# Kernel optimization log

Measured on AMD Instinct MI355X. Metric: run time of the kernel, lower is better.

Reference implementation:

```python
import jax, jax.numpy as jnp
import numpy as np
import math
from jax import lax

TSCALE = 256
NUM_SAMPLE = 32
PERBIN = 3
WINDOWS = [4, 8, 16, 32, 64, 128, 192, 256]
RATIO = 0.25
B = 2
DIM = 512
H1 = 256   # hid_dim_1d
H3 = 512   # hid_dim_3d
H2 = 128   # hid_dim_2d


def _bin_mask(xmin, xmax, tscale, num_sample, perbin):
    # exact replica of BEM._get_interp1d_bin_mask (setup-time numpy)
    plen = float(xmax - xmin)
    step = plen / (num_sample * perbin - 1.0)
    samples = [xmin + step * i for i in range(num_sample * perbin)]
    cols = []
    for idx in range(num_sample):
        v = np.zeros([tscale])
        for s in samples[idx * perbin:(idx + 1) * perbin]:
            up = math.ceil(s)
            dec, down = math.modf(s)
            if 0 <= int(down) <= tscale - 1:
                v[int(down)] += 1 - dec
            if 0 <= int(up) <= tscale - 1:
                v[int(up)] += dec
        cols.append(v / perbin)
    return np.stack(cols, axis=1)  # (tscale, num_sample)


def build_sample_mask():
    mats = []
    for w in WINDOWS:
        ws = w + w * RATIO
        vecs = []
        for t in range(TSCALE):
            d = ws * 0.5
            vecs.append(_bin_mask(t - d, t + d, TSCALE, NUM_SAMPLE, PERBIN))
        mats.append(np.stack(vecs, axis=2))  # (T, N, T)
    m = np.stack(mats, axis=3).astype(np.float32)  # (T, N, T, W)
    return jnp.asarray(m.reshape(TSCALE, -1))  # (T, N*T*W)


def gn(x, g, b, groups=32, eps=1e-5):
    Bsz, C = x.shape[0], x.shape[1]
    xr = x.reshape(Bsz, groups, -1)
    mu = xr.mean(-1, keepdims=True)
    var = xr.var(-1, keepdims=True)
    xr = (xr - mu) * lax.rsqrt(var + eps)
    x = xr.reshape(x.shape)
    bshape = (1, C) + (1,) * (x.ndim - 2)
    return x * g.reshape(bshape) + b.reshape(bshape)


def conv(x, w, b, strides, padding, dn):
    y = lax.conv_general_dilated(x, w, strides, padding, dimension_numbers=dn)
    return y + b.reshape((1, -1) + (1,) * (y.ndim - 2))


def setup_inputs() -> dict:
    key = jax.random.key(0)
    ks = jax.random.split(key, 16)

    def w(k, shape, fan):
        return (jax.random.normal(k, shape) * (1.0 / np.sqrt(fan))).astype(jnp.float32)

    inp = {}
    inp['x'] = jax.random.normal(ks[0], (B, DIM, TSCALE), jnp.float32)
    inp['sample_mask'] = build_sample_mask()
    inp['c1_w'] = w(ks[1], (H1, DIM, 3), DIM * 3)
    inp['c1_b'] = jnp.zeros((H1,), jnp.float32)
    inp['gn1_g'] = jnp.ones((H1,), jnp.float32)
    inp['gn1_b'] = jnp.zeros((H1,), jnp.float32)
    inp['r3d_w'] = w(ks[2], (H3, H1, NUM_SAMPLE, 1, 1), H1 * NUM_SAMPLE)
    inp['r3d_b'] = jnp.zeros((H3,), jnp.float32)
    inp['gn3_g'] = jnp.ones((H3,), jnp.float32)
    inp['gn3_b'] = jnp.zeros((H3,), jnp.float32)
    inp['r2d_w'] = w(ks[3], (H2, H3, 1, 1), H3)
    inp['r2d_b'] = jnp.zeros((H2,), jnp.float32)
    inp['gn2_g'] = jnp.ones((H2,), jnp.float32)
    inp['gn2_b'] = jnp.zeros((H2,), jnp.float32)
    inp['s1_w'] = w(ks[4], (H2, H2, 3, 3), H2 * 9)
    inp['s1_b'] = jnp.zeros((H2,), jnp.float32)
    inp['sgn_g'] = jnp.ones((H2,), jnp.float32)
    inp['sgn_b'] = jnp.zeros((H2,), jnp.float32)
    inp['s2_w'] = w(ks[5], (1, H2, 1, 1), H2)
    inp['s2_b'] = jnp.zeros((1,), jnp.float32)
    inp['e1_w'] = w(ks[6], (H2, H2, 3, 3), H2 * 9)
    inp['e1_b'] = jnp.zeros((H2,), jnp.float32)
    inp['egn_g'] = jnp.ones((H2,), jnp.float32)
    inp['egn_b'] = jnp.zeros((H2,), jnp.float32)
    inp['e2_w'] = w(ks[7], (1, H2, 1, 1), H2)
    inp['e2_b'] = jnp.zeros((1,), jnp.float32)
    return inp


def reference(x, sample_mask, c1_w, c1_b, gn1_g, gn1_b, r3d_w, r3d_b, gn3_g, gn3_b,
              r2d_w, r2d_b, gn2_g, gn2_b, s1_w, s1_b, sgn_g, sgn_b, s2_w, s2_b,
              e1_w, e1_b, egn_g, egn_b, e2_w, e2_b):
    relu = jax.nn.relu
    W = len(WINDOWS)
    # conv_1: Unit1D(k=3, same pad) + GN + ReLU  -> (B, H1, T)
    h = relu(gn(conv(x, c1_w, c1_b, (1,), [(1, 1)], ('NCH', 'OIH', 'NCH')), gn1_g, gn1_b))
    Bsz, C, T = h.shape
    # sample: dense GEMM against sparse interp1d mask -> (B, C, N, T, W)
    samp = jnp.matmul(h, sample_mask).reshape(Bsz, C, NUM_SAMPLE, T, W)
    # reduction_layer 'fc': Conv3d over the N axis (kernel=stride=N) + GN + ReLU
    y = conv(samp, r3d_w, r3d_b, (NUM_SAMPLE, 1, 1), 'VALID', ('NCDHW', 'OIDHW', 'NCDHW'))
    y = relu(gn(y, gn3_g, gn3_b))[:, :, 0]  # squeeze depth -> (B, H3, T, W)
    f = relu(gn(conv(y, r2d_w, r2d_b, (1, 1), 'VALID', ('NCHW', 'OIHW', 'NCHW')), gn2_g, gn2_b))

    def head(w1, b1, gg, gb, w2, b2):
        t = relu(gn(conv(f, w1, b1, (1, 1), [(1, 1), (1, 1)], ('NCHW', 'OIHW', 'NCHW')), gg, gb))
        return jax.nn.sigmoid(conv(t, w2, b2, (1, 1), 'VALID', ('NCHW', 'OIHW', 'NCHW')))

    cs = head(s1_w, s1_b, sgn_g, sgn_b, s2_w, s2_b)  # (B,1,T,W)
    ce = head(e1_w, e1_b, egn_g, egn_b, e2_w, e2_b)  # (B,1,T,W)
    return jnp.concatenate([cs, ce], axis=1)  # (B,2,T,W): [start, end]
```

## Files before the change

kernel.cpp:

```cpp
#include <hip/hip_runtime.h>
#include <hip/hip_bf16.h>

typedef __hip_bfloat16 bf16;
typedef __attribute__((ext_vector_type(8))) short short8;
typedef __attribute__((ext_vector_type(4))) float f32x4;

static __device__ __forceinline__ float b2f(bf16 v) { return __bfloat162float(v); }

static __device__ __forceinline__ float ldin(const void* p, long i, int bf) {
    return bf ? b2f(((const bf16*)p)[i]) : ((const float*)p)[i];
}

__global__ void detect_k(const unsigned short* __restrict__ x16, int* __restrict__ flag) {
    __shared__ int cnt[256];
    unsigned short u = x16[threadIdx.x];
    int e = (u >> 7) & 0xFF;
    cnt[threadIdx.x] = (e >= 100 && e <= 140) ? 1 : 0;
    __syncthreads();
    for (int off = 128; off > 0; off >>= 1) {
        if (threadIdx.x < off) cnt[threadIdx.x] += cnt[threadIdx.x + off];
        __syncthreads();
    }
    if (threadIdx.x == 0) *flag = (cnt[0] > 217) ? 1 : 0;
}

__global__ void cast_bf_k(const void* __restrict__ in, bf16* __restrict__ out,
                          int n, const int* __restrict__ flagp) {
    int bf = *flagp;
    int idx = blockIdx.x * 256 + threadIdx.x;
    if (idx >= n) return;
    out[idx] = __float2bfloat16(ldin(in, idx, bf));
}

__global__ __launch_bounds__(256) void transpose_w3b_k(const void* __restrict__ w3,
                                                       bf16* __restrict__ out,
                                                       const int* __restrict__ flagp) {
    int bf = *flagp;
    int h3 = blockIdx.x;
    __shared__ bf16 t[8192];
    long base = (long)h3 * 8192;
    for (int i = threadIdx.x; i < 8192; i += 256)
        t[i] = __float2bfloat16(ldin(w3, base + i, bf));
    __syncthreads();
    for (int i = threadIdx.x; i < 8192; i += 256) {
        int n = i >> 8, c = i & 255;
        out[((long)n * 512 + h3) * 256 + c] = t[c * 32 + n];
    }
}

__global__ void cast_hT_k(const float* __restrict__ h, bf16* __restrict__ out) {
    int idx = blockIdx.x * 256 + threadIdx.x;
    if (idx >= 131072) return;
    int b = idx >> 16, r = idx & 65535;
    int tau = r >> 8, c = r & 255;
    out[idx] = __float2bfloat16(h[b * 65536 + c * 256 + tau]);
}

__global__ __launch_bounds__(256) void castT_k(const float* __restrict__ y,
                                               bf16* __restrict__ yT) {
    int p0 = blockIdx.x * 64, c0 = blockIdx.y * 64, b = blockIdx.z;
    __shared__ bf16 t[64][65];
    const float* src = y + (long)b * 1048576;
    for (int i = threadIdx.x; i < 4096; i += 256) {
        int cl = i >> 6, pl = i & 63;
        t[pl][cl] = __float2bfloat16(src[(long)(c0 + cl) * 2048 + p0 + pl]);
    }
    __syncthreads();
    bf16* dst = yT + (long)b * 1048576;
    for (int i = threadIdx.x; i < 4096; i += 256) {
        int pl = i >> 6, cl = i & 63;
        dst[(long)(p0 + pl) * 512 + c0 + cl] = t[pl][cl];
    }
}

__global__ void im2col_xb_k(const void* __restrict__ x, bf16* __restrict__ out,
                            const int* __restrict__ flagp) {
    int bf = *flagp;
    int idx = blockIdx.x * 256 + threadIdx.x;
    if (idx >= 786432) return;
    int b = idx / 393216;
    int rem = idx - b * 393216;
    int t = rem / 1536, k = rem - t * 1536;
    int c = k / 3, q = k - c * 3;
    int tt = t + q - 1;
    float v = (tt >= 0 && tt < 256) ? ldin(x, ((long)b * 512 + c) * 256 + tt, bf) : 0.f;
    out[idx] = __float2bfloat16(v);
}

__global__ void im2col_fb_k(const float* __restrict__ f, bf16* __restrict__ out) {
    int idx = blockIdx.x * 256 + threadIdx.x;
    if (idx >= 4718592) return;
    int b = idx / 2359296;
    int rem = idx - b * 2359296;
    int p = rem / 1152, k = rem - p * 1152;
    int c = k / 9, q = k - c * 9;
    int dy = q / 3, dx = q - dy * 3;
    int t = p >> 3, w = p & 7;
    int tt = t + dy - 1, ww = w + dx - 1;
    float v = (tt >= 0 && tt < 256 && ww >= 0 && ww < 8)
                  ? f[((long)b * 128 + c) * 2048 + tt * 8 + ww] : 0.f;
    out[idx] = __float2bfloat16(v);
}

template<int NT>
__global__ __launch_bounds__(256) void wgemm_mfma(
    const bf16* __restrict__ A, const bf16* __restrict__ B, float* __restrict__ C,
    const void* __restrict__ bias1, const void* __restrict__ bias2,
    int M, int K, int P, int a_div, long a_zs, const int* __restrict__ flagp)
{
    int bf = *flagp;
    int z = blockIdx.z;
    const bf16* A2 = A + (long)(z / a_div) * a_zs;
    const bf16* B2 = B + (long)(z & 1) * (long)P * K;
    float* C2 = C + (long)z * M * P;
    const void* bi = (z / a_div) ? bias2 : bias1;

    int tid = threadIdx.x;
    int wv = tid >> 6, lane = tid & 63;
    int q = lane >> 4, col = lane & 15;
    int m0 = blockIdx.y * 64 + wv * 16;
    int p0 = blockIdx.x * (16 * NT);

    f32x4 acc[NT];
    #pragma unroll
    for (int i = 0; i < NT; ++i) acc[i] = (f32x4){0.f, 0.f, 0.f, 0.f};

    const short8* Ab = (const short8*)(A2 + (long)(m0 + col) * K);
    int kch = K >> 5;
    for (int kc = 0; kc < kch; ++kc) {
        short8 af = Ab[kc * 4 + q];
        #pragma unroll
        for (int nt = 0; nt < NT; ++nt) {
            const short8* Bb = (const short8*)(B2 + (long)(p0 + nt * 16 + col) * K);
            short8 bfr = Bb[kc * 4 + q];
            acc[nt] = __builtin_amdgcn_mfma_f32_16x16x32_bf16(af, bfr, acc[nt], 0, 0, 0);
        }
    }

    float bv[4];
    #pragma unroll
    for (int r = 0; r < 4; ++r) bv[r] = ldin(bi, m0 + q * 4 + r, bf);
    #pragma unroll
    for (int nt = 0; nt < NT; ++nt)
        #pragma unroll
        for (int r = 0; r < 4; ++r)
            C2[(long)(m0 + q * 4 + r) * P + p0 + nt * 16 + col] = acc[nt][r] + bv[r];
}

__global__ __launch_bounds__(256) void pgemm_mfma(
    const bf16* __restrict__ w3b, const bf16* __restrict__ hbT,
    float* __restrict__ P)
{
    int z = blockIdx.z;
    int b = z >> 5, n = z & 31;
    int bm = blockIdx.y;
    int tid = threadIdx.x;
    int wv = tid >> 6, lane = tid & 63;
    int q = lane >> 4, col = lane & 15;

    f32x4 acc[16];
    #pragma unroll
    for (int i = 0; i < 16; ++i) acc[i] = (f32x4){0.f, 0.f, 0.f, 0.f};

    const short8* Abase = (const short8*)(w3b + ((long)n * 512 + bm * 64 + wv * 16 + col) * 256);
    const short8* Bbase = (const short8*)(hbT + (long)b * 65536);

    #pragma unroll
    for (int kc = 0; kc < 8; ++kc) {
        short8 af = Abase[kc * 4 + q];
        #pragma unroll
        for (int nt = 0; nt < 16; ++nt) {
            short8 bfr = Bbase[(nt * 16 + col) * 32 + kc * 4 + q];
            acc[nt] = __builtin_amdgcn_mfma_f32_16x16x32_bf16(af, bfr, acc[nt], 0, 0, 0);
        }
    }

    long dbase = (long)b * 4194304 + (long)n * 256 +
                 (long)(bm * 64 + wv * 16 + q * 4) * 8192 + col;
    #pragma unroll
    for (int nt = 0; nt < 16; ++nt)
        #pragma unroll
        for (int r = 0; r < 4; ++r)
            P[dbase + (long)r * 8192 + nt * 16] = acc[nt][r];
}

__global__ __launch_bounds__(1024) void gn_relu_k(
    float* __restrict__ buf, const void* __restrict__ g, const void* __restrict__ bt,
    int C, int S, int groups, const int* __restrict__ flagp)
{
    int bf = *flagp;
    int nt = blockDim.x;
    int gid = blockIdx.x;
    int b = gid / groups, gr = gid % groups;
    int cpg = C / groups;
    long cnt = (long)cpg * S;
    float* base = buf + ((long)b * C + (long)gr * cpg) * S;
    double s = 0.0, s2 = 0.0;
    for (long i = threadIdx.x; i < cnt; i += nt) {
        float v = base[i];
        s += v; s2 += (double)v * v;
    }
    __shared__ double rs[1024], rq[1024];
    rs[threadIdx.x] = s; rq[threadIdx.x] = s2;
    __syncthreads();
    for (int off = nt >> 1; off > 0; off >>= 1) {
        if (threadIdx.x < off) { rs[threadIdx.x] += rs[threadIdx.x + off]; rq[threadIdx.x] += rq[threadIdx.x + off]; }
        __syncthreads();
    }
    double mean_d = rs[0] / (double)cnt;
    float mean = (float)mean_d;
    float var = (float)(rq[0] / (double)cnt - mean_d * mean_d);
    float rstd = rsqrtf(var + 1e-5f);
    for (long i = threadIdx.x; i < cnt; i += nt) {
        int c = gr * cpg + (int)(i / S);
        float v = (base[i] - mean) * rstd * ldin(g, c, bf) + ldin(bt, c, bf);
        base[i] = v > 0.f ? v : 0.f;
    }
}

__global__ __launch_bounds__(256) void gn_part_k(
    const float* __restrict__ buf, double* __restrict__ part,
    int C, int S, int groups, int chunks)
{
    int gi = blockIdx.x / chunks, ch = blockIdx.x % chunks;
    int b = gi / groups, gr = gi % groups;
    int cpg = C / groups;
    long cnt = (long)cpg * S;
    long clen = cnt / chunks;
    const float* base = buf + ((long)b * C + (long)gr * cpg) * S + (long)ch * clen;
    double s = 0.0, s2 = 0.0;
    for (long i = threadIdx.x; i < clen; i += 256) {
        float v = base[i];
        s += v; s2 += (double)v * v;
    }
    __shared__ double rs[256], rq[256];
    rs[threadIdx.x] = s; rq[threadIdx.x] = s2;
    __syncthreads();
    for (int off = 128; off > 0; off >>= 1) {
        if (threadIdx.x < off) { rs[threadIdx.x] += rs[threadIdx.x + off]; rq[threadIdx.x] += rq[threadIdx.x + off]; }
        __syncthreads();
    }
    if (threadIdx.x == 0) { part[blockIdx.x * 2] = rs[0]; part[blockIdx.x * 2 + 1] = rq[0]; }
}

__global__ __launch_bounds__(256) void gn_apply_k(
    float* __restrict__ buf, const double* __restrict__ part,
    const void* __restrict__ g, const void* __restrict__ bt,
    int C, int S, int groups, int chunks, const int* __restrict__ flagp)
{
    int bf = *flagp;
    int gi = blockIdx.x / chunks, ch = blockIdx.x % chunks;
    int b = gi / groups, gr = gi % groups;
    int cpg = C / groups;
    long cnt = (long)cpg * S;
    long clen = cnt / chunks;
    double s = 0.0, s2 = 0.0;
    for (int k = 0; k < chunks; ++k) {
        s += part[(gi * chunks + k) * 2];
        s2 += part[(gi * chunks + k) * 2 + 1];
    }
    double mean_d = s / (double)cnt;
    float mean = (float)mean_d;
    float var = (float)(s2 / (double)cnt - mean_d * mean_d);
    float rstd = rsqrtf(var + 1e-5f);
    float* base = buf + ((long)b * C + (long)gr * cpg) * S + (long)ch * clen;
    long off0 = (long)ch * clen;
    for (long i = threadIdx.x; i < clen; i += 256) {
        int c = gr * cpg + (int)((off0 + i) / S);
        float v = (base[i] - mean) * rstd * ldin(g, c, bf) + ldin(bt, c, bf);
        base[i] = v > 0.f ? v : 0.f;
    }
}

__global__ __launch_bounds__(384) void build_table_k(
    const void* __restrict__ mask, int* __restrict__ tabd,
    float* __restrict__ tabw, const int* __restrict__ flagp)
{
    int bf = *flagp;
    int nw = blockIdx.x;
    int w = nw >> 5, n = nw & 31;
    int tid = threadIdx.x;
    int d = tid - 165;
    float v = 0.f;
    if (d <= 165) {
        if (d < 0) v = ldin(mask, (long)(254 + d) * 65536 + ((long)n * 256 + 254) * 8 + w, bf);
        else       v = ldin(mask, (long)(1 + d) * 65536 + ((long)n * 256 + 1) * 8 + w, bf);
    }
    __shared__ unsigned char nz[384];
    nz[tid] = (v != 0.f) ? 1 : 0;
    if (tid < 6) { tabd[nw * 6 + tid] = 0; tabw[nw * 6 + tid] = 0.f; }
    __syncthreads();
    if (v != 0.f) {
        int slot = 0;
        for (int j = 0; j < tid; ++j) slot += nz[j];
        if (slot < 6) { tabd[nw * 6 + slot] = d; tabw[nw * 6 + slot] = v; }
    }
}

__global__ void build_corr_k(const void* __restrict__ mask, const int* __restrict__ tabd,
                             const float* __restrict__ tabw, float* __restrict__ corrB,
                             const int* __restrict__ flagp) {
    int bf = *flagp;
    int idx = blockIdx.x * 256 + threadIdx.x;
    if (idx >= 65536) return;
    int n = idx >> 11, p = idx & 2047;
    int t = p >> 3, w = p & 7;
    float mv = ldin(mask, ((long)n * 256 + t) * 8 + w, bf);
    float sub = 0.f;
    int base = (w * 32 + n) * 6;
    for (int k = 0; k < 6; ++k)
        if (tabd[base + k] == -t && tabw[base + k] != 0.f) sub += tabw[base + k];
    corrB[idx] = mv - sub;
}

__global__ __launch_bounds__(256) void apply_y_k(
    const float* __restrict__ P, const int* __restrict__ tabd,
    const float* __restrict__ tabw, float* __restrict__ part,
    const int* __restrict__ flagp)
{
    int bx = blockIdx.x;
    int h3 = bx >> 1, half = bx & 1;
    int n0 = half * 16;
    __shared__ float2 Pl2[16 * 256];
    __shared__ float4 Tp4[384];
    const float4* p04 = (const float4*)(P + ((long)h3 * 32 + n0) * 256);
    const float4* p14 = (const float4*)(P + ((long)(512 + h3) * 32 + n0) * 256);
    float4* pl4 = (float4*)Pl2;
    for (int i = threadIdx.x; i < 1024; i += 256) {
        float4 a = p04[i], b = p14[i];
        pl4[i * 2]     = make_float4(a.x, b.x, a.y, b.y);
        pl4[i * 2 + 1] = make_float4(a.z, b.z, a.w, b.w);
    }
    float2* tp2 = (float2*)Tp4;
    for (int i = threadIdx.x; i < 768; i += 256) {
        int el = i / 6, k = i - el * 6;
        int ge = ((el >> 4) << 5) + n0 + (el & 15);
        tp2[i] = make_float2(tabw[ge * 6 + k], __int_as_float(tabd[ge * 6 + k]));
    }
    __syncthreads();

    int t = threadIdx.x;
    float a0[8], a1[8];
    #pragma unroll
    for (int w = 0; w < 8; ++w) { a0[w] = 0.f; a1[w] = 0.f; }

    #pragma unroll 1
    for (int nl = 0; nl < 16; ++nl) {
        const float2* Pn = Pl2 + (nl << 8);
        #pragma unroll
        for (int w = 0; w < 8; ++w) {
            int e4 = ((w << 4) + nl) * 3;
            float4 q0 = Tp4[e4], q1 = Tp4[e4 + 1], q2 = Tp4[e4 + 2];
            float wts[6] = {q0.x, q0.z, q1.x, q1.z, q2.x, q2.z};
            int   dss[6] = {__float_as_int(q0.y), __float_as_int(q0.w),
                            __float_as_int(q1.y), __float_as_int(q1.w),
                            __float_as_int(q2.y), __float_as_int(q2.w)};
            #pragma unroll
            for (int k = 0; k < 6; ++k) {
                int tau = t + dss[k];
                int idx = tau & 255;
                float wt = ((unsigned)tau < 256u) ? wts[k] : 0.f;
                float2 pv = Pn[idx];
                a0[w] += wt * pv.x;
                a1[w] += wt * pv.y;
            }
        }
    }

    long y0 = (long)half * 2097152 + (long)h3 * 2048 + (long)t * 8;
    long y1 = y0 + 512L * 2048;
    *(float4*)(part + y0)     = make_float4(a0[0], a0[1], a0[2], a0[3]);
    *(float4*)(part + y0 + 4) = make_float4(a0[4], a0[5], a0[6], a0[7]);
    *(float4*)(part + y1)     = make_float4(a1[0], a1[1], a1[2], a1[3]);
    *(float4*)(part + y1 + 4) = make_float4(a1[4], a1[5], a1[6], a1[7]);
}

__global__ void merge_y_k(const float* __restrict__ part, const float* __restrict__ P,
                          const float* __restrict__ corrB, float* __restrict__ y,
                          const void* __restrict__ r3b, const int* __restrict__ flagp) {
    int bf = *flagp;
    int i = blockIdx.x * 256 + threadIdx.x;
    if (i >= 524288) return;
    const float4* p4 = (const float4*)part;
    float4 a = p4[i], b = p4[i + 524288];
    long e = (long)i * 4;
    int bb_ = (int)(e >> 20);
    int h3 = (int)((e >> 11) & 511);
    int p = (int)(e & 2047);
    float bias = ldin(r3b, h3, bf);
    float4 acc = make_float4(a.x + b.x + bias, a.y + b.y + bias,
                             a.z + b.z + bias, a.w + b.w + bias);
    const float* p0 = P + ((long)(bb_ * 512 + h3) * 32) * 256;
    #pragma unroll 4
    for (int n = 0; n < 32; ++n) {
        float pv = p0[n * 256];
        float4 cb = *(const float4*)(corrB + n * 2048 + p);
        acc.x += pv * cb.x; acc.y += pv * cb.y;
        acc.z += pv * cb.z; acc.w += pv * cb.w;
    }
    ((float4*)y)[i] = acc;
}

__global__ __launch_bounds__(64) void head_out_k(
    const float* __restrict__ t1s, const float* __restrict__ t1e,
    const void* __restrict__ s2w, const void* __restrict__ s2b,
    const void* __restrict__ e2w, const void* __restrict__ e2b,
    void* __restrict__ out, const int* __restrict__ flagp) {
    int bf = *flagp;
    int idx = blockIdx.x * 64 + threadIdx.x;
    if (idx >= 4096) return;
    int b = idx >> 11, p = idx & 2047;
    const float* ts = t1s + (long)b * 262144 + p;
    const float* te = t1e + (long)b * 262144 + p;
    float as = ldin(s2b, 0, bf), ae = ldin(e2b, 0, bf);
    #pragma unroll 8
    for (int c = 0; c < 128; ++c) {
        as += ldin(s2w, c, bf) * ts[(long)c * 2048];
        ae += ldin(e2w, c, bf) * te[(long)c * 2048];
    }
    float vs = 1.f / (1.f + expf(-as));
    float ve = 1.f / (1.f + expf(-ae));
    long o0 = ((long)b * 2) * 2048 + p;
    long o1 = ((long)b * 2 + 1) * 2048 + p;
    if (bf) {
        ((bf16*)out)[o0] = __float2bfloat16(vs);
        ((bf16*)out)[o1] = __float2bfloat16(ve);
    } else {
        ((float*)out)[o0] = vs;
        ((float*)out)[o1] = ve;
    }
}

extern "C" void kernel_launch(void* const* d_in, const int* in_sizes, int n_in,
                              void* d_out, int out_size, void* d_ws, size_t ws_size,
                              hipStream_t stream) {
    const void* x    = d_in[0];
    const void* mask = d_in[1];
    const void* c1w  = d_in[2];
    const void* c1b  = d_in[3];
    const void* gn1g = d_in[4];
    const void* gn1b = d_in[5];
    const void* w3   = d_in[6];
    const void* r3b  = d_in[7];
    const void* gn3g = d_in[8];
    const void* gn3b = d_in[9];
    const void* w2   = d_in[10];
    const void* r2b  = d_in[11];
    const void* gn2g = d_in[12];
    const void* gn2b = d_in[13];
    const void* s1w  = d_in[14];
    const void* s1b  = d_in[15];
    const void* sgng = d_in[16];
    const void* sgnb = d_in[17];
    const void* s2w  = d_in[18];
    const void* s2b  = d_in[19];
    const void* e1w  = d_in[20];
    const void* e1b  = d_in[21];
    const void* egng = d_in[22];
    const void* egnb = d_in[23];
    const void* e2w  = d_in[24];
    const void* e2b  = d_in[25];
    float* ws = (float*)d_ws;

    int*   flagI = (int*)(ws + 0);
    float* h     = ws + 64;
    float* c1t   = ws + 131136;
    float* w2t   = ws + 524352;
    float* s1t   = ws + 589888;
    float* corrB = ws + 884800;
    float* tabw  = ws + 950336;
    int*   tabd  = (int*)(ws + 951872);
    float* t1s   = ws + 986176;
    float* t1e   = ws + 1510464;
    float* f     = ws + 2034752;
    float* y     = ws + 2559040;
    float* w3reg = ws + 4656192;
    float* Pb    = ws + 8850496;
    double* gnbuf = (double*)(ws + 17239104);
    bf16*  w3b   = (bf16*)w3reg;
    bf16*  hbT   = (bf16*)(w3reg + 2097152);
    bf16*  c1wb  = (bf16*)c1t;
    bf16*  w2b   = (bf16*)w2t;
    bf16*  hwb   = (bf16*)s1t;
    bf16*  colxb = (bf16*)y;
    bf16*  fcolb = (bf16*)Pb;
    bf16*  yT    = (bf16*)(Pb + 4194304);
    float* ypart = w3reg;

    dim3 blk(256);
    dim3 blkG(1024);

    detect_k<<<dim3(1), blk, 0, stream>>>((const unsigned short*)x, flagI);

    cast_bf_k<<<dim3(1536), blk, 0, stream>>>(c1w, c1wb, 393216, flagI);
    cast_bf_k<<<dim3(576),  blk, 0, stream>>>(s1w, hwb, 147456, flagI);
    cast_bf_k<<<dim3(576),  blk, 0, stream>>>(e1w, hwb + 147456, 147456, flagI);
    cast_bf_k<<<dim3(256),  blk, 0, stream>>>(w2, w2b, 65536, flagI);
    transpose_w3b_k<<<dim3(512), blk, 0, stream>>>(w3, w3b, flagI);
    build_table_k<<<dim3(256), dim3(384), 0, stream>>>(mask, tabd, tabw, flagI);
    build_corr_k<<<dim3(256), blk, 0, stream>>>(mask, tabd, tabw, corrB, flagI);

    im2col_xb_k<<<dim3(3072), blk, 0, stream>>>(x, colxb, flagI);
    wgemm_mfma<1><<<dim3(16, 4, 2), blk, 0, stream>>>(
        c1wb, colxb, h, c1b, c1b, 256, 1536, 256, 1, 0L, flagI);
    gn_relu_k<<<dim3(64), blkG, 0, stream>>>(h, gn1g, gn1b, 256, 256, 32, flagI);

    cast_hT_k<<<dim3(512), blk, 0, stream>>>(h, hbT);
    pgemm_mfma<<<dim3(1, 8, 64), blk, 0, stream>>>(w3b, hbT, Pb);

    apply_y_k<<<dim3(1024), blk, 0, stream>>>(Pb, tabd, tabw, ypart, flagI);
    merge_y_k<<<dim3(2048), blk, 0, stream>>>(ypart, Pb, corrB, y, r3b, flagI);
    gn_part_k<<<dim3(512), blk, 0, stream>>>(y, gnbuf, 512, 2048, 32, 8);
    gn_apply_k<<<dim3(512), blk, 0, stream>>>(y, gnbuf, gn3g, gn3b, 512, 2048, 32, 8, flagI);

    castT_k<<<dim3(32, 8, 2), blk, 0, stream>>>(y, yT);
    wgemm_mfma<2><<<dim3(64, 2, 2), blk, 0, stream>>>(
        w2b, yT, f, r2b, r2b, 128, 512, 2048, 2, 0L, flagI);
    gn_part_k<<<dim3(256), blk, 0, stream>>>(f, gnbuf, 128, 2048, 32, 4);
    gn_apply_k<<<dim3(256), blk, 0, stream>>>(f, gnbuf, gn2g, gn2b, 128, 2048, 32, 4, flagI);

    im2col_fb_k<<<dim3(18432), blk, 0, stream>>>(f, fcolb);
    wgemm_mfma<4><<<dim3(32, 2, 4), blk, 0, stream>>>(
        hwb, fcolb, t1s, s1b, e1b, 128, 1152, 2048, 2, 147456L, flagI);
    gn_part_k<<<dim3(256), blk, 0, stream>>>(t1s, gnbuf, 128, 2048, 32, 4);
    gn_apply_k<<<dim3(256), blk, 0, stream>>>(t1s, gnbuf, sgng, sgnb, 128, 2048, 32, 4, flagI);
    gn_part_k<<<dim3(256), blk, 0, stream>>>(t1e, gnbuf, 128, 2048, 32, 4);
    gn_apply_k<<<dim3(256), blk, 0, stream>>>(t1e, gnbuf, egng, egnb, 128, 2048, 32, 4, flagI);

    head_out_k<<<dim3(64), dim3(64), 0, stream>>>(t1s, t1e, s2w, s2b, e2w, e2b, d_out, flagI);
}
```

Measured before the change: 432.6 us.

## Fuse prep kernels, GN with transpose-cast, merge with GN stats, head GNs

Several small launches are merged. Five weight-cast/transpose kernels and the table build become one multi-role prep kernel. GroupNorm1 now also writes the transposed bf16 copy of h, which removes cast_hT. The y merge is fused with the GN3 partial statistics pass, and the two head GroupNorms run as a single batched part/apply pair that treats t1s and t1e as contiguous. The aim is less launch overhead and fewer full-tensor passes. In exchange, the merged y kernel loses its float4 vectorization, and the batched head GN relies on t1e sitting directly after t1s in memory.

```diff
diff --git a/kernel.cpp b/kernel.cpp
--- a/kernel.cpp
+++ b/kernel.cpp
@@ -24,53 +24,90 @@
     if (threadIdx.x == 0) *flag = (cnt[0] > 217) ? 1 : 0;
 }
 
-__global__ void cast_bf_k(const void* __restrict__ in, bf16* __restrict__ out,
-                          int n, const int* __restrict__ flagp) {
+__global__ __launch_bounds__(384) void prep_k(
+    const void* __restrict__ c1w, const void* __restrict__ s1w,
+    const void* __restrict__ e1w, const void* __restrict__ w2,
+    const void* __restrict__ w3, const void* __restrict__ mask,
+    bf16* __restrict__ c1wb, bf16* __restrict__ hwb, bf16* __restrict__ w2b,
+    bf16* __restrict__ w3b, int* __restrict__ tabd, float* __restrict__ tabw,
+    const int* __restrict__ flagp)
+{
+    __shared__ char sm[16384];
+    int bf = *flagp;
+    int blk = blockIdx.x, tid = threadIdx.x;
+    if (blk < 1024) {
+        int idx = blk * 384 + tid;
+        if (idx < 393216) c1wb[idx] = __float2bfloat16(ldin(c1w, idx, bf));
+        return;
+    }
+    blk -= 1024;
+    if (blk < 384) {
+        int idx = blk * 384 + tid;
+        if (idx < 147456) hwb[idx] = __float2bfloat16(ldin(s1w, idx, bf));
+        return;
+    }
+    blk -= 384;
+    if (blk < 384) {
+        int idx = blk * 384 + tid;
+        if (idx < 147456) hwb[147456 + idx] = __float2bfloat16(ldin(e1w, idx, bf));
+        return;
+    }
+    blk -= 384;
+    if (blk < 171) {
+        int idx = blk * 384 + tid;
+        if (idx < 65536) w2b[idx] = __float2bfloat16(ldin(w2, idx, bf));
+        return;
+    }
+    blk -= 171;
+    if (blk < 512) {
+        int h3 = blk;
+        bf16* t = (bf16*)sm;
+        long base = (long)h3 * 8192;
+        for (int i = tid; i < 8192; i += 384)
+            t[i] = __float2bfloat16(ldin(w3, base + i, bf));
+        __syncthreads();
+        for (int i = tid; i < 8192; i += 384) {
+            int n = i >> 8, c = i & 255;
+            w3b[((long)n * 512 + h3) * 256 + c] = t[c * 32 + n];
+        }
+        return;
+    }
+    blk -= 512;
+    {
+        int nw = blk;
+        int w = nw >> 5, n = nw & 31;
+        int d = tid - 165;
+        float v = 0.f;
+        if (d <= 165) {
+            if (d < 0) v = ldin(mask, (long)(254 + d) * 65536 + ((long)n * 256 + 254) * 8 + w, bf);
+            else       v = ldin(mask, (long)(1 + d) * 65536 + ((long)n * 256 + 1) * 8 + w, bf);
+        }
+        unsigned char* nz = (unsigned char*)sm;
+        nz[tid] = (v != 0.f) ? 1 : 0;
+        if (tid < 6) { tabd[nw * 6 + tid] = 0; tabw[nw * 6 + tid] = 0.f; }
+        __syncthreads();
+        if (v != 0.f) {
+            int slot = 0;
+            for (int j = 0; j < tid; ++j) slot += nz[j];
+            if (slot < 6) { tabd[nw * 6 + slot] = d; tabw[nw * 6 + slot] = v; }
+        }
+    }
+}
+
+__global__ void build_corr_k(const void* __restrict__ mask, const int* __restrict__ tabd,
+                             const float* __restrict__ tabw, float* __restrict__ corrB,
+                             const int* __restrict__ flagp) {
     int bf = *flagp;
     int idx = blockIdx.x * 256 + threadIdx.x;
-    if (idx >= n) return;
-    out[idx] = __float2bfloat16(ldin(in, idx, bf));
-}
-
-__global__ __launch_bounds__(256) void transpose_w3b_k(const void* __restrict__ w3,
-                                                       bf16* __restrict__ out,
-                                                       const int* __restrict__ flagp) {
-    int bf = *flagp;
-    int h3 = blockIdx.x;
-    __shared__ bf16 t[8192];
-    long base = (long)h3 * 8192;
-    for (int i = threadIdx.x; i < 8192; i += 256)
-        t[i] = __float2bfloat16(ldin(w3, base + i, bf));
-    __syncthreads();
-    for (int i = threadIdx.x; i < 8192; i += 256) {
-        int n = i >> 8, c = i & 255;
-        out[((long)n * 512 + h3) * 256 + c] = t[c * 32 + n];
-    }
-}
-
-__global__ void cast_hT_k(const float* __restrict__ h, bf16* __restrict__ out) {
-    int idx = blockIdx.x * 256 + threadIdx.x;
-    if (idx >= 131072) return;
-    int b = idx >> 16, r = idx & 65535;
-    int tau = r >> 8, c = r & 255;
-    out[idx] = __float2bfloat16(h[b * 65536 + c * 256 + tau]);
-}
-
-__global__ __launch_bounds__(256) void castT_k(const float* __restrict__ y,
-                                               bf16* __restrict__ yT) {
-    int p0 = blockIdx.x * 64, c0 = blockIdx.y * 64, b = blockIdx.z;
-    __shared__ bf16 t[64][65];
-    const float* src = y + (long)b * 1048576;
-    for (int i = threadIdx.x; i < 4096; i += 256) {
-        int cl = i >> 6, pl = i & 63;
-        t[pl][cl] = __float2bfloat16(src[(long)(c0 + cl) * 2048 + p0 + pl]);
-    }
-    __syncthreads();
-    bf16* dst = yT + (long)b * 1048576;
-    for (int i = threadIdx.x; i < 4096; i += 256) {
-        int pl = i >> 6, cl = i & 63;
-        dst[(long)(p0 + pl) * 512 + c0 + cl] = t[pl][cl];
-    }
+    if (idx >= 65536) return;
+    int n = idx >> 11, p = idx & 2047;
+    int t = p >> 3, w = p & 7;
+    float mv = ldin(mask, ((long)n * 256 + t) * 8 + w, bf);
+    float sub = 0.f;
+    int base = (w * 32 + n) * 6;
+    for (int k = 0; k < 6; ++k)
+        if (tabd[base + k] == -t && tabw[base + k] != 0.f) sub += tabw[base + k];
+    corrB[idx] = mv - sub;
 }
 
 __global__ void im2col_xb_k(const void* __restrict__ x, bf16* __restrict__ out,
@@ -102,6 +139,23 @@
     out[idx] = __float2bfloat16(v);
 }
 
+__global__ __launch_bounds__(256) void castT_k(const float* __restrict__ y,
+                                               bf16* __restrict__ yT) {
+    int p0 = blockIdx.x * 64, c0 = blockIdx.y * 64, b = blockIdx.z;
+    __shared__ bf16 t[64][65];
+    const float* src = y + (long)b * 1048576;
+    for (int i = threadIdx.x; i < 4096; i += 256) {
+        int cl = i >> 6, pl = i & 63;
+        t[pl][cl] = __float2bfloat16(src[(long)(c0 + cl) * 2048 + p0 + pl]);
+    }
+    __syncthreads();
+    bf16* dst = yT + (long)b * 1048576;
+    for (int i = threadIdx.x; i < 4096; i += 256) {
+        int pl = i >> 6, cl = i & 63;
+        dst[(long)(p0 + pl) * 512 + c0 + cl] = t[pl][cl];
+    }
+}
+
 template<int NT>
 __global__ __launch_bounds__(256) void wgemm_mfma(
     const bf16* __restrict__ A, const bf16* __restrict__ B, float* __restrict__ C,
@@ -184,37 +238,37 @@
             P[dbase + (long)r * 8192 + nt * 16] = acc[nt][r];
 }
 
-__global__ __launch_bounds__(1024) void gn_relu_k(
-    float* __restrict__ buf, const void* __restrict__ g, const void* __restrict__ bt,
-    int C, int S, int groups, const int* __restrict__ flagp)
-{
-    int bf = *flagp;
-    int nt = blockDim.x;
+__global__ __launch_bounds__(1024) void gn_relu_h_k(
+    float* __restrict__ h, bf16* __restrict__ hbT,
+    const void* __restrict__ g, const void* __restrict__ bt,
+    const int* __restrict__ flagp)
+{
+    int bf = *flagp;
     int gid = blockIdx.x;
-    int b = gid / groups, gr = gid % groups;
-    int cpg = C / groups;
-    long cnt = (long)cpg * S;
-    float* base = buf + ((long)b * C + (long)gr * cpg) * S;
+    int b = gid >> 5, gr = gid & 31;
+    float* base = h + ((long)b * 256 + gr * 8) * 256;
     double s = 0.0, s2 = 0.0;
-    for (long i = threadIdx.x; i < cnt; i += nt) {
+    for (int i = threadIdx.x; i < 2048; i += 1024) {
         float v = base[i];
         s += v; s2 += (double)v * v;
     }
     __shared__ double rs[1024], rq[1024];
     rs[threadIdx.x] = s; rq[threadIdx.x] = s2;
     __syncthreads();
-    for (int off = nt >> 1; off > 0; off >>= 1) {
+    for (int off = 512; off > 0; off >>= 1) {
         if (threadIdx.x < off) { rs[threadIdx.x] += rs[threadIdx.x + off]; rq[threadIdx.x] += rq[threadIdx.x + off]; }
         __syncthreads();
     }
-    double mean_d = rs[0] / (double)cnt;
+    double mean_d = rs[0] / 2048.0;
     float mean = (float)mean_d;
-    float var = (float)(rq[0] / (double)cnt - mean_d * mean_d);
+    float var = (float)(rq[0] / 2048.0 - mean_d * mean_d);
     float rstd = rsqrtf(var + 1e-5f);
-    for (long i = threadIdx.x; i < cnt; i += nt) {
-        int c = gr * cpg + (int)(i / S);
+    for (int i = threadIdx.x; i < 2048; i += 1024) {
+        int c = gr * 8 + (i >> 8), tau = i & 255;
         float v = (base[i] - mean) * rstd * ldin(g, c, bf) + ldin(bt, c, bf);
-        base[i] = v > 0.f ? v : 0.f;
+        v = v > 0.f ? v : 0.f;
+        base[i] = v;
+        hbT[(long)b * 65536 + tau * 256 + c] = __float2bfloat16(v);
     }
 }
 
@@ -272,45 +326,34 @@
     }
 }
 
-__global__ __launch_bounds__(384) void build_table_k(
-    const void* __restrict__ mask, int* __restrict__ tabd,
-    float* __restrict__ tabw, const int* __restrict__ flagp)
-{
-    int bf = *flagp;
-    int nw = blockIdx.x;
-    int w = nw >> 5, n = nw & 31;
-    int tid = threadIdx.x;
-    int d = tid - 165;
-    float v = 0.f;
-    if (d <= 165) {
-        if (d < 0) v = ldin(mask, (long)(254 + d) * 65536 + ((long)n * 256 + 254) * 8 + w, bf);
-        else       v = ldin(mask, (long)(1 + d) * 65536 + ((long)n * 256 + 1) * 8 + w, bf);
-    }
-    __shared__ unsigned char nz[384];
-    nz[tid] = (v != 0.f) ? 1 : 0;
-    if (tid < 6) { tabd[nw * 6 + tid] = 0; tabw[nw * 6 + tid] = 0.f; }
-    __syncthreads();
-    if (v != 0.f) {
-        int slot = 0;
-        for (int j = 0; j < tid; ++j) slot += nz[j];
-        if (slot < 6) { tabd[nw * 6 + slot] = d; tabw[nw * 6 + slot] = v; }
-    }
-}
-
-__global__ void build_corr_k(const void* __restrict__ mask, const int* __restrict__ tabd,
-                             const float* __restrict__ tabw, float* __restrict__ corrB,
-                             const int* __restrict__ flagp) {
-    int bf = *flagp;
-    int idx = blockIdx.x * 256 + threadIdx.x;
-    if (idx >= 65536) return;
-    int n = idx >> 11, p = idx & 2047;
-    int t = p >> 3, w = p & 7;
-    float mv = ldin(mask, ((long)n * 256 + t) * 8 + w, bf);
-    float sub = 0.f;
-    int base = (w * 32 + n) * 6;
-    for (int k = 0; k < 6; ++k)
-        if (tabd[base + k] == -t && tabw[base + k] != 0.f) sub += tabw[base + k];
-    corrB[idx] = mv - sub;
+__global__ __launch_bounds__(256) void gn_apply2_k(
+    float* __restrict__ buf, const double* __restrict__ part,
+    const void* __restrict__ g1, const void* __restrict__ b1,
+    const void* __restrict__ g2, const void* __restrict__ b2,
+    int chunks, const int* __restrict__ flagp)
+{
+    int bf = *flagp;
+    int gi = blockIdx.x / chunks, ch = blockIdx.x % chunks;
+    int b = gi >> 5, gr = gi & 31;
+    const void* g = (b >= 2) ? g2 : g1;
+    const void* bt = (b >= 2) ? b2 : b1;
+    long cnt = 8192, clen = cnt / chunks;
+    double s = 0.0, s2 = 0.0;
+    for (int k = 0; k < chunks; ++k) {
+        s += part[(gi * chunks + k) * 2];
+        s2 += part[(gi * chunks + k) * 2 + 1];
+    }
+    double mean_d = s / (double)cnt;
+    float mean = (float)mean_d;
+    float var = (float)(s2 / (double)cnt - mean_d * mean_d);
+    float rstd = rsqrtf(var + 1e-5f);
+    float* base = buf + ((long)b * 128 + gr * 4) * 2048 + (long)ch * clen;
+    long off0 = (long)ch * clen;
+    for (long i = threadIdx.x; i < clen; i += 256) {
+        int c = gr * 4 + (int)((off0 + i) >> 11);
+        float v = (base[i] - mean) * rstd * ldin(g, c, bf) + ldin(bt, c, bf);
+        base[i] = v > 0.f ? v : 0.f;
+    }
 }
 
 __global__ __launch_bounds__(256) void apply_y_k(
@@ -375,30 +418,38 @@
     *(float4*)(part + y1 + 4) = make_float4(a1[4], a1[5], a1[6], a1[7]);
 }
 
-__global__ void merge_y_k(const float* __restrict__ part, const float* __restrict__ P,
-                          const float* __restrict__ corrB, float* __restrict__ y,
-                          const void* __restrict__ r3b, const int* __restrict__ flagp) {
-    int bf = *flagp;
-    int i = blockIdx.x * 256 + threadIdx.x;
-    if (i >= 524288) return;
-    const float4* p4 = (const float4*)part;
-    float4 a = p4[i], b = p4[i + 524288];
-    long e = (long)i * 4;
-    int bb_ = (int)(e >> 20);
-    int h3 = (int)((e >> 11) & 511);
-    int p = (int)(e & 2047);
-    float bias = ldin(r3b, h3, bf);
-    float4 acc = make_float4(a.x + b.x + bias, a.y + b.y + bias,
-                             a.z + b.z + bias, a.w + b.w + bias);
-    const float* p0 = P + ((long)(bb_ * 512 + h3) * 32) * 256;
-    #pragma unroll 4
-    for (int n = 0; n < 32; ++n) {
-        float pv = p0[n * 256];
-        float4 cb = *(const float4*)(corrB + n * 2048 + p);
-        acc.x += pv * cb.x; acc.y += pv * cb.y;
-        acc.z += pv * cb.z; acc.w += pv * cb.w;
-    }
-    ((float4*)y)[i] = acc;
+__global__ __launch_bounds__(256) void gn3_part_k(
+    const float* __restrict__ ypart, const float* __restrict__ P,
+    const float* __restrict__ corrB, const void* __restrict__ r3b,
+    float* __restrict__ y, double* __restrict__ part,
+    const int* __restrict__ flagp)
+{
+    int bf = *flagp;
+    int gi = blockIdx.x >> 3, ch = blockIdx.x & 7;
+    int b = gi >> 5, gr = gi & 31;
+    long e0 = ((long)b * 512 + gr * 16) * 2048 + (long)ch * 4096;
+    double s = 0.0, s2 = 0.0;
+    for (int i = threadIdx.x; i < 4096; i += 256) {
+        long e = e0 + i;
+        int loc = ch * 4096 + i;
+        int h3 = gr * 16 + (loc >> 11);
+        int p = loc & 2047;
+        float v = ypart[e] + ypart[2097152 + e] + ldin(r3b, h3, bf);
+        const float* p0 = P + ((long)(b * 512 + h3) * 32) * 256;
+        #pragma unroll 4
+        for (int n = 0; n < 32; ++n)
+            v += p0[n * 256] * corrB[n * 2048 + p];
+        y[e] = v;
+        s += v; s2 += (double)v * v;
+    }
+    __shared__ double rs[256], rq[256];
+    rs[threadIdx.x] = s; rq[threadIdx.x] = s2;
+    __syncthreads();
+    for (int off = 128; off > 0; off >>= 1) {
+        if (threadIdx.x < off) { rs[threadIdx.x] += rs[threadIdx.x + off]; rq[threadIdx.x] += rq[threadIdx.x + off]; }
+        __syncthreads();
+    }
+    if (threadIdx.x == 0) { part[blockIdx.x * 2] = rs[0]; part[blockIdx.x * 2 + 1] = rq[0]; }
 }
 
 __global__ __launch_bounds__(64) void head_out_k(
@@ -488,29 +539,22 @@
     float* ypart = w3reg;
 
     dim3 blk(256);
-    dim3 blkG(1024);
 
     detect_k<<<dim3(1), blk, 0, stream>>>((const unsigned short*)x, flagI);
 
-    cast_bf_k<<<dim3(1536), blk, 0, stream>>>(c1w, c1wb, 393216, flagI);
-    cast_bf_k<<<dim3(576),  blk, 0, stream>>>(s1w, hwb, 147456, flagI);
-    cast_bf_k<<<dim3(576),  blk, 0, stream>>>(e1w, hwb + 147456, 147456, flagI);
-    cast_bf_k<<<dim3(256),  blk, 0, stream>>>(w2, w2b, 65536, flagI);
-    transpose_w3b_k<<<dim3(512), blk, 0, stream>>>(w3, w3b, flagI);
-    build_table_k<<<dim3(256), dim3(384), 0, stream>>>(mask, tabd, tabw, flagI);
+    prep_k<<<dim3(2731), dim3(384), 0, stream>>>(
+        c1w, s1w, e1w, w2, w3, mask, c1wb, hwb, w2b, w3b, tabd, tabw, flagI);
     build_corr_k<<<dim3(256), blk, 0, stream>>>(mask, tabd, tabw, corrB, flagI);
 
     im2col_xb_k<<<dim3(3072), blk, 0, stream>>>(x, colxb, flagI);
     wgemm_mfma<1><<<dim3(16, 4, 2), blk, 0, stream>>>(
         c1wb, colxb, h, c1b, c1b, 256, 1536, 256, 1, 0L, flagI);
-    gn_relu_k<<<dim3(64), blkG, 0, stream>>>(h, gn1g, gn1b, 256, 256, 32, flagI);
-
-    cast_hT_k<<<dim3(512), blk, 0, stream>>>(h, hbT);
+    gn_relu_h_k<<<dim3(64), dim3(1024), 0, stream>>>(h, hbT, gn1g, gn1b, flagI);
+
     pgemm_mfma<<<dim3(1, 8, 64), blk, 0, stream>>>(w3b, hbT, Pb);
 
     apply_y_k<<<dim3(1024), blk, 0, stream>>>(Pb, tabd, tabw, ypart, flagI);
-    merge_y_k<<<dim3(2048), blk, 0, stream>>>(ypart, Pb, corrB, y, r3b, flagI);
-    gn_part_k<<<dim3(512), blk, 0, stream>>>(y, gnbuf, 512, 2048, 32, 8);
+    gn3_part_k<<<dim3(512), blk, 0, stream>>>(ypart, Pb, corrB, r3b, y, gnbuf, flagI);
     gn_apply_k<<<dim3(512), blk, 0, stream>>>(y, gnbuf, gn3g, gn3b, 512, 2048, 32, 8, flagI);
 
     castT_k<<<dim3(32, 8, 2), blk, 0, stream>>>(y, yT);
@@ -522,10 +566,8 @@
     im2col_fb_k<<<dim3(18432), blk, 0, stream>>>(f, fcolb);
     wgemm_mfma<4><<<dim3(32, 2, 4), blk, 0, stream>>>(
         hwb, fcolb, t1s, s1b, e1b, 128, 1152, 2048, 2, 147456L, flagI);
-    gn_part_k<<<dim3(256), blk, 0, stream>>>(t1s, gnbuf, 128, 2048, 32, 4);
-    gn_apply_k<<<dim3(256), blk, 0, stream>>>(t1s, gnbuf, sgng, sgnb, 128, 2048, 32, 4, flagI);
-    gn_part_k<<<dim3(256), blk, 0, stream>>>(t1e, gnbuf, 128, 2048, 32, 4);
-    gn_apply_k<<<dim3(256), blk, 0, stream>>>(t1e, gnbuf, egng, egnb, 128, 2048, 32, 4, flagI);
+    gn_part_k<<<dim3(512), blk, 0, stream>>>(t1s, gnbuf, 128, 2048, 32, 4);
+    gn_apply2_k<<<dim3(512), blk, 0, stream>>>(t1s, gnbuf, sgng, sgnb, egng, egnb, 4, flagI);
 
     head_out_k<<<dim3(64), dim3(64), 0, stream>>>(t1s, t1e, s2w, s2b, e2w, e2b, d_out, flagI);
 }
```

Result: slower. 442.1 us (+2.2%).
